# Performance work log

Hardware: AMD Instinct MI355X
Metric: run time of the kernel (lower is better)

## Reference

```python
import jax, jax.numpy as jnp
import numpy as np
import math

SR = 44100  # sampling_rate from init_kwargs


def setup_inputs() -> dict:
    key = jax.random.key(0)
    k1, k2, k3, k4 = jax.random.split(key, 4)
    B, T, C = 32, 262144, 1024
    x = jax.random.normal(k1, (B, T), jnp.float32)
    # rescale uniform [0,1) to realistic formant parameter ranges
    freq = jax.random.uniform(k2, (B, C), jnp.float32) * 3800.0 + 200.0  # Hz
    bw = jax.random.uniform(k3, (B, C), jnp.float32) * 400.0 + 50.0      # Hz
    gain = jax.random.uniform(k4, (B, C), jnp.float32) + 0.1
    return {"x": x, "freq": freq, "bw": bw, "gain": gain}


def _coeffs(freq, bw, gain, T):
    """Vectorized per-sample biquad coefficients via linear interpolation of controls."""
    nyquist = SR / 2
    fn = jnp.clip(freq / nyquist, 1e-5, 0.95)  # [B, C]
    bn = jnp.clip(bw / nyquist, 1e-5, 0.95)
    C = freq.shape[1]
    t = jnp.arange(T, dtype=jnp.float32)
    cf = t / (T / C)                      # control-rate fractional index per sample
    idx = jnp.floor(cf).astype(jnp.int32)
    frac = cf - idx                       # [T]
    nxt = jnp.minimum(idx + 1, C - 1)

    def interp(v):  # [B,C] -> [B,T]
        return v[:, idx] * (1.0 - frac) + v[:, nxt] * frac

    f_t = interp(fn)
    b_t = interp(bn)
    g_t = interp(gain)
    omega = (2.0 * math.pi) * f_t
    sin_w = jnp.sin(omega)
    cos_w = jnp.cos(omega)
    alpha = sin_w * jnp.sinh((math.log(2.0) / 2.0) * b_t * omega / sin_w)
    a0 = 1.0 + alpha
    b0 = alpha * g_t / a0
    b2 = -alpha * g_t / a0   # b1 == 0, term dropped
    a1 = -2.0 * cos_w / a0
    a2 = (1.0 - alpha) / a0
    return b0, b2, a1, a2    # each [B, T]


def reference(x, freq, bw, gain):
    B, T = x.shape
    b0, b2, a1, a2 = _coeffs(freq, bw, gain, T)

    def step(carry, inp):
        y1, y2, x1, x2 = carry
        xt, b0t, b2t, a1t, a2t = inp
        y = b0t * xt + b2t * x2 - a1t * y1 - a2t * y2
        return (y, y1, xt, x1), y

    z = jnp.zeros((B,), x.dtype)
    seq = (x.T, b0.T, b2.T, a1.T, a2.T)  # each [T, B]
    (y1, y2, x1, x2), ys = jax.lax.scan(step, (z, z, z, z), seq)
    return ys.T, (y1, y2, x1, x2)
```

## Files before the change

kernel.cpp:

```cpp
#include <hip/hip_runtime.h>
#include <hip/hip_bf16.h>

#define BB 32
#define TT 262144
#define CC 1024
#define LL 32
#define THREADS 256
#define BLKROW 32
#define NBLK (BB*BLKROW)
#define NT (NBLK*THREADS)
#define SPB (THREADS*LL)
#define PIDX(l) ((((l)>>5)*33) + ((l)&31))

__device__ __forceinline__ float clipn(float v){
  return fminf(fmaxf(v, 1e-5f), 0.95f);
}

__device__ __forceinline__ void coef(float fn, float bn, float gt,
                                     float& b0c, float& p1, float& p2){
  float cw = __builtin_amdgcn_cosf(fn);
  float alpha = 2.1775860903036022f * bn * fn;
  float inv = __builtin_amdgcn_rcpf(1.0f + alpha);
  b0c = alpha*gt*inv;
  p1  = 2.0f*cw*inv;
  p2  = (alpha - 1.0f)*inv;
}

__device__ __forceinline__ void ctrl(const float* __restrict__ fqp,
                                     const float* __restrict__ bwp,
                                     const float* __restrict__ gnp,
                                     int b, int t0,
                                     float& f0, float& df, float& w0, float& dw,
                                     float& g0, float& dg, float& fr0){
  int idx = t0 >> 8;
  int nx  = idx + 1 < CC ? idx + 1 : CC - 1;
  const float inyq = 1.0f/22050.0f;
  int cb = b*CC;
  f0 = clipn(fqp[cb+idx]*inyq);
  float f1 = clipn(fqp[cb+nx]*inyq);
  w0 = clipn(bwp[cb+idx]*inyq);
  float w1 = clipn(bwp[cb+nx]*inyq);
  g0 = gnp[cb+idx];
  float g1 = gnp[cb+nx];
  df = f1-f0; dw = w1-w0; dg = g1-g0;
  fr0 = (float)(t0 & 255) * (1.0f/256.0f);
}

__device__ __forceinline__ void segMapLds(const float* xrow, float xs2, float xs1,
                                          float f0,float df,float w0,float dw,
                                          float g0,float dg,float fr0,
                                          float& m00,float& m01,float& m10,float& m11,
                                          float& v0,float& v1){
  m00=1.f;m01=0.f;m10=0.f;m11=1.f;v0=0.f;v1=0.f;
  float xm2 = xs2, xm1 = xs1;
#pragma unroll
  for (int j=0;j<LL;++j){
    float frac = fr0 + (float)j*(1.0f/256.0f);
    float b0c,p1,p2;
    coef(f0+df*frac, w0+dw*frac, g0+dg*frac, b0c, p1, p2);
    float xc = xrow[j];
    float w = b0c*(xc - xm2);
    float n00 = p1*m00 + p2*m10;
    float n01 = p1*m01 + p2*m11;
    float nv0 = p1*v0 + p2*v1 + w;
    m10=m00; m11=m01; m00=n00; m01=n01;
    v1=v0; v0=nv0;
    xm2=xm1; xm1=xc;
  }
}

__device__ __forceinline__ void waveScan(int lane,
    float& m00,float& m01,float& m10,float& m11,float& v0,float& v1){
#pragma unroll
  for (int d=1; d<64; d<<=1){
    float p00=__shfl_up(m00,(unsigned)d,64), p01=__shfl_up(m01,(unsigned)d,64),
          p10=__shfl_up(m10,(unsigned)d,64), p11=__shfl_up(m11,(unsigned)d,64),
          pv0=__shfl_up(v0,(unsigned)d,64),  pv1=__shfl_up(v1,(unsigned)d,64);
    if (lane >= d){
      float n00=m00*p00+m01*p10, n01=m00*p01+m01*p11;
      float n10=m10*p00+m11*p10, n11=m10*p01+m11*p11;
      float nv0=m00*pv0+m01*pv1+v0, nv1=m10*pv0+m11*pv1+v1;
      m00=n00;m01=n01;m10=n10;m11=n11;v0=nv0;v1=nv1;
    }
  }
}

__device__ __forceinline__ void stageIn(const float* __restrict__ src, float* tile, int tid){
  const float4* s4 = reinterpret_cast<const float4*>(src);
#pragma unroll
  for (int k=0;k<8;++k){
    float4 v = s4[tid + k*256];
    int p = PIDX((tid + k*256)*4);
    tile[p]=v.x; tile[p+1]=v.y; tile[p+2]=v.z; tile[p+3]=v.w;
  }
}

__global__ __launch_bounds__(THREADS) void mapScan(
    const float* __restrict__ x, const float* __restrict__ fqp,
    const float* __restrict__ bwp, const float* __restrict__ gnp,
    float* __restrict__ ws){
  __shared__ float tile[THREADS*33];
  __shared__ float wagg[4][6];
  const int blkId = blockIdx.x;
  const int row = blkId >> 5;
  const int blk = blkId & 31;
  const int tid = threadIdx.x;
  const int lane = tid & 63;
  const int wid = tid >> 6;
  const int g = blkId*THREADS + tid;
  const int t0 = blk*SPB + tid*LL;
  const float* xb = x + (size_t)row*TT;

  stageIn(xb + blk*SPB, tile, tid);

  float f0,df,w0,dw,g0,dg,fr0;
  ctrl(fqp,bwp,gnp,row,t0,f0,df,w0,dw,g0,dg,fr0);
  __syncthreads();

  float xs1, xs2;
  if (tid > 0){
    xs1 = tile[(tid-1)*33 + 31];
    xs2 = tile[(tid-1)*33 + 30];
  } else if (blk > 0){
    xs1 = xb[blk*SPB - 1];
    xs2 = xb[blk*SPB - 2];
  } else { xs1 = 0.f; xs2 = 0.f; }

  float m00,m01,m10,m11,v0,v1;
  segMapLds(tile + tid*33, xs2, xs1, f0,df,w0,dw,g0,dg,fr0, m00,m01,m10,m11,v0,v1);

  waveScan(lane, m00,m01,m10,m11,v0,v1);
  if (lane == 63){
    wagg[wid][0]=m00; wagg[wid][1]=m01; wagg[wid][2]=m10;
    wagg[wid][3]=m11; wagg[wid][4]=v0;  wagg[wid][5]=v1;
  }
  float e00=__shfl_up(m00,1u,64), e01=__shfl_up(m01,1u,64),
        e10=__shfl_up(m10,1u,64), e11=__shfl_up(m11,1u,64),
        ev0=__shfl_up(v0,1u,64),  ev1=__shfl_up(v1,1u,64);
  if (lane == 0){ e00=1.f;e01=0.f;e10=0.f;e11=1.f;ev0=0.f;ev1=0.f; }
  __syncthreads();

  float W00=1.f,W01=0.f,W10=0.f,W11=1.f,Wv0=0.f,Wv1=0.f;
  for (int w=0; w<wid; ++w){
    float A0=wagg[w][0],A1=wagg[w][1],A2=wagg[w][2],
          A3=wagg[w][3],A4=wagg[w][4],A5=wagg[w][5];
    float n00=A0*W00+A1*W10, n01=A0*W01+A1*W11;
    float n10=A2*W00+A3*W10, n11=A2*W01+A3*W11;
    float nv0=A0*Wv0+A1*Wv1+A4, nv1=A2*Wv0+A3*Wv1+A5;
    W00=n00;W01=n01;W10=n10;W11=n11;Wv0=nv0;Wv1=nv1;
  }
  float F00 = e00*W00 + e01*W10, F01 = e00*W01 + e01*W11;
  float F10 = e10*W00 + e11*W10, F11 = e10*W01 + e11*W11;
  float Fv0 = e00*Wv0 + e01*Wv1 + ev0;
  float Fv1 = e10*Wv0 + e11*Wv1 + ev1;

  float2* fw = reinterpret_cast<float2*>(ws);
  fw[0*NT + g] = make_float2(F00, F01);
  fw[1*NT + g] = make_float2(F10, F11);
  fw[2*NT + g] = make_float2(Fv0, Fv1);

  if (tid == 0){
    float B00=1.f,B01=0.f,B10=0.f,B11=1.f,Bv0=0.f,Bv1=0.f;
#pragma unroll
    for (int w=0; w<4; ++w){
      float A0=wagg[w][0],A1=wagg[w][1],A2=wagg[w][2],
            A3=wagg[w][3],A4=wagg[w][4],A5=wagg[w][5];
      float n00=A0*B00+A1*B10, n01=A0*B01+A1*B11;
      float n10=A2*B00+A3*B10, n11=A2*B01+A3*B11;
      float nv0=A0*Bv0+A1*Bv1+A4, nv1=A2*Bv0+A3*Bv1+A5;
      B00=n00;B01=n01;B10=n10;B11=n11;Bv0=nv0;Bv1=nv1;
    }
    float* aggf = ws + (size_t)6*NT + blkId*6;
    aggf[0]=B00; aggf[1]=B01; aggf[2]=B10; aggf[3]=B11; aggf[4]=Bv0; aggf[5]=Bv1;
  }
}

__global__ __launch_bounds__(THREADS) void replay(
    const float* __restrict__ x, const float* __restrict__ fqp,
    const float* __restrict__ bwp, const float* __restrict__ gnp,
    const float* __restrict__ ws, float* __restrict__ out){
  __shared__ float tile[THREADS*33];
  __shared__ float svb[2];
  const int blkId = blockIdx.x;
  const int row = blkId >> 5;
  const int blk = blkId & 31;
  const int tid = threadIdx.x;
  const int g = blkId*THREADS + tid;
  const int t0 = blk*SPB + tid*LL;
  const float* xb = x + (size_t)row*TT;

  stageIn(xb + blk*SPB, tile, tid);

  float f0,df,w0,dw,g0,dg,fr0;
  ctrl(fqp,bwp,gnp,row,t0,f0,df,w0,dw,g0,dg,fr0);

  const float2* fw = reinterpret_cast<const float2*>(ws);
  float2 q0 = fw[0*NT + g];
  float2 q1 = fw[1*NT + g];
  float2 q2 = fw[2*NT + g];
  float F00=q0.x, F01=q0.y, F10=q1.x, F11=q1.y, Fv0=q2.x, Fv1=q2.y;

  if (tid < 32){
    const float* aggf = ws + (size_t)6*NT + (row*32 + tid)*6;
    float A0=aggf[0],A1=aggf[1],A2=aggf[2],A3=aggf[3],A4=aggf[4],A5=aggf[5];
#pragma unroll
    for (int d=1; d<32; d<<=1){
      float p00=__shfl_up(A0,(unsigned)d,32), p01=__shfl_up(A1,(unsigned)d,32),
            p10=__shfl_up(A2,(unsigned)d,32), p11=__shfl_up(A3,(unsigned)d,32),
            pv0=__shfl_up(A4,(unsigned)d,32), pv1=__shfl_up(A5,(unsigned)d,32);
      if (tid >= d){
        float n00=A0*p00+A1*p10, n01=A0*p01+A1*p11;
        float n10=A2*p00+A3*p10, n11=A2*p01+A3*p11;
        float nv0=A0*pv0+A1*pv1+A4, nv1=A2*pv0+A3*pv1+A5;
        A0=n00;A1=n01;A2=n10;A3=n11;A4=nv0;A5=nv1;
      }
    }
    float pv0 = 0.f, pv1 = 0.f;
    if (blk > 0){
      pv0 = __shfl(A4, blk-1, 32);
      pv1 = __shfl(A5, blk-1, 32);
    }
    if (tid==0){ svb[0]=pv0; svb[1]=pv1; }
  }
  __syncthreads();

  float xs1, xs2;
  if (tid > 0){
    xs1 = tile[(tid-1)*33 + 31];
    xs2 = tile[(tid-1)*33 + 30];
  } else if (blk > 0){
    xs1 = xb[blk*SPB - 1];
    xs2 = xb[blk*SPB - 2];
  } else { xs1 = 0.f; xs2 = 0.f; }

  float bv0 = svb[0], bv1 = svb[1];
  float y1 = F00*bv0 + F01*bv1 + Fv0;
  float y2 = F10*bv0 + F11*bv1 + Fv1;

  float* xrow = tile + tid*33;
  float xm2 = xs2, xm1 = xs1;
#pragma unroll
  for (int j=0;j<LL;++j){
    float frac = fr0 + (float)j*(1.0f/256.0f);
    float b0c,p1,p2;
    coef(f0+df*frac, w0+dw*frac, g0+dg*frac, b0c, p1, p2);
    float xc = xrow[j];
    float y = b0c*(xc - xm2) + p1*y1 + p2*y2;
    xrow[j] = y;
    y2=y1; y1=y;
    xm2=xm1; xm1=xc;
  }
  __syncthreads();

  float* ob = out + (size_t)row*TT + blk*SPB;
  float4* o4 = reinterpret_cast<float4*>(ob);
#pragma unroll
  for (int k=0;k<8;++k){
    int p = PIDX((tid + k*256)*4);
    o4[tid + k*256] = make_float4(tile[p], tile[p+1], tile[p+2], tile[p+3]);
  }
  if (blk==31 && tid==THREADS-1){
    size_t base = (size_t)BB*TT;
    out[base + row]        = y1;
    out[base + BB + row]   = y2;
    out[base + 2*BB + row] = xm1;
    out[base + 3*BB + row] = xm2;
  }
}

extern "C" void kernel_launch(void* const* d_in, const int* in_sizes, int n_in,
                              void* d_out, int out_size, void* d_ws, size_t ws_size,
                              hipStream_t stream) {
  const float* x  = (const float*)d_in[0];
  const float* fq = (const float*)d_in[1];
  const float* bw = (const float*)d_in[2];
  const float* gn = (const float*)d_in[3];
  float* out = (float*)d_out;
  float* ws  = (float*)d_ws;

  hipLaunchKernelGGL(mapScan, dim3(NBLK), dim3(THREADS), 0, stream, x, fq, bw, gn, ws);
  hipLaunchKernelGGL(replay,  dim3(NBLK), dim3(THREADS), 0, stream, x, fq, bw, gn, ws, out);
}
```

Before: 31.70 us.

## Load x directly into registers in mapScan, reorder loads, use nontemporal stores

```diff
diff --git a/kernel.cpp b/kernel.cpp
--- a/kernel.cpp
+++ b/kernel.cpp
@@ -11,6 +11,8 @@
 #define NT (NBLK*THREADS)
 #define SPB (THREADS*LL)
 #define PIDX(l) ((((l)>>5)*33) + ((l)&31))
+
+typedef float f32x4 __attribute__((ext_vector_type(4)));
 
 __device__ __forceinline__ float clipn(float v){
   return fminf(fmaxf(v, 1e-5f), 0.95f);
@@ -46,7 +48,7 @@
   fr0 = (float)(t0 & 255) * (1.0f/256.0f);
 }
 
-__device__ __forceinline__ void segMapLds(const float* xrow, float xs2, float xs1,
+__device__ __forceinline__ void segMapReg(const float* xr, float xs2, float xs1,
                                           float f0,float df,float w0,float dw,
                                           float g0,float dg,float fr0,
                                           float& m00,float& m01,float& m10,float& m11,
@@ -58,7 +60,7 @@
     float frac = fr0 + (float)j*(1.0f/256.0f);
     float b0c,p1,p2;
     coef(f0+df*frac, w0+dw*frac, g0+dg*frac, b0c, p1, p2);
-    float xc = xrow[j];
+    float xc = xr[j];
     float w = b0c*(xc - xm2);
     float n00 = p1*m00 + p2*m10;
     float n01 = p1*m01 + p2*m11;
@@ -99,7 +101,6 @@
     const float* __restrict__ x, const float* __restrict__ fqp,
     const float* __restrict__ bwp, const float* __restrict__ gnp,
     float* __restrict__ ws){
-  __shared__ float tile[THREADS*33];
   __shared__ float wagg[4][6];
   const int blkId = blockIdx.x;
   const int row = blkId >> 5;
@@ -111,23 +112,27 @@
   const int t0 = blk*SPB + tid*LL;
   const float* xb = x + (size_t)row*TT;
 
-  stageIn(xb + blk*SPB, tile, tid);
+  float xr[LL];
+  {
+    const float4* xv = reinterpret_cast<const float4*>(xb + t0);
+#pragma unroll
+    for (int q=0;q<LL/4;++q){
+      float4 v = xv[q];
+      xr[4*q]=v.x; xr[4*q+1]=v.y; xr[4*q+2]=v.z; xr[4*q+3]=v.w;
+    }
+  }
+  float xs1 = __shfl_up(xr[31], 1u, 64);
+  float xs2 = __shfl_up(xr[30], 1u, 64);
+  if (lane == 0){
+    if (t0 > 0){ xs1 = xb[t0-1]; xs2 = xb[t0-2]; }
+    else       { xs1 = 0.f;      xs2 = 0.f; }
+  }
 
   float f0,df,w0,dw,g0,dg,fr0;
   ctrl(fqp,bwp,gnp,row,t0,f0,df,w0,dw,g0,dg,fr0);
-  __syncthreads();
-
-  float xs1, xs2;
-  if (tid > 0){
-    xs1 = tile[(tid-1)*33 + 31];
-    xs2 = tile[(tid-1)*33 + 30];
-  } else if (blk > 0){
-    xs1 = xb[blk*SPB - 1];
-    xs2 = xb[blk*SPB - 2];
-  } else { xs1 = 0.f; xs2 = 0.f; }
 
   float m00,m01,m10,m11,v0,v1;
-  segMapLds(tile + tid*33, xs2, xs1, f0,df,w0,dw,g0,dg,fr0, m00,m01,m10,m11,v0,v1);
+  segMapReg(xr, xs2, xs1, f0,df,w0,dw,g0,dg,fr0, m00,m01,m10,m11,v0,v1);
 
   waveScan(lane, m00,m01,m10,m11,v0,v1);
   if (lane == 63){
@@ -189,15 +194,16 @@
   const int t0 = blk*SPB + tid*LL;
   const float* xb = x + (size_t)row*TT;
 
-  stageIn(xb + blk*SPB, tile, tid);
-
-  float f0,df,w0,dw,g0,dg,fr0;
-  ctrl(fqp,bwp,gnp,row,t0,f0,df,w0,dw,g0,dg,fr0);
-
   const float2* fw = reinterpret_cast<const float2*>(ws);
   float2 q0 = fw[0*NT + g];
   float2 q1 = fw[1*NT + g];
   float2 q2 = fw[2*NT + g];
+
+  stageIn(xb + blk*SPB, tile, tid);
+
+  float f0,df,w0,dw,g0,dg,fr0;
+  ctrl(fqp,bwp,gnp,row,t0,f0,df,w0,dw,g0,dg,fr0);
+
   float F00=q0.x, F01=q0.y, F10=q1.x, F11=q1.y, Fv0=q2.x, Fv1=q2.y;
 
   if (tid < 32){
@@ -253,11 +259,12 @@
   __syncthreads();
 
   float* ob = out + (size_t)row*TT + blk*SPB;
-  float4* o4 = reinterpret_cast<float4*>(ob);
+  f32x4* o4 = reinterpret_cast<f32x4*>(ob);
 #pragma unroll
   for (int k=0;k<8;++k){
     int p = PIDX((tid + k*256)*4);
-    o4[tid + k*256] = make_float4(tile[p], tile[p+1], tile[p+2], tile[p+3]);
+    f32x4 v = { tile[p], tile[p+1], tile[p+2], tile[p+3] };
+    __builtin_nontemporal_store(v, &o4[tid + k*256]);
   }
   if (blk==31 && tid==THREADS-1){
     size_t base = (size_t)BB*TT;
```

Result: faster. 29.82 us (median of 2 runs) (-5.9%).
